# Kernel optimization log

Hardware: AMD Instinct MI355X
Metric: run time of the kernel (lower is better)

## Reference

```python
import jax, jax.numpy as jnp
import numpy as np


def setup_inputs() -> dict:
    key = jax.random.key(0)
    k1, k2 = jax.random.split(key)
    input_tensor = jax.random.normal(k1, (32, 128, 64, 64), dtype=jnp.float32)
    weights = jax.random.normal(k2, (256, 128, 3, 3), dtype=jnp.float32) * 0.05
    return {"input_tensor": input_tensor, "weights": weights}


def reference(input_tensor, weights):
    # Valid-padding, stride-1, no-bias direct conv2d (NCHW x OIHW -> NCHW),
    # identical math to the quintuple-loop slice*weight sum in the original.
    return jax.lax.conv_general_dilated(
        input_tensor,
        weights,
        window_strides=(1, 1),
        padding="VALID",
        dimension_numbers=("NCHW", "OIHW", "NCHW"),
    )
```

## Files before the change

kernel.cpp:

```cpp
#include <hip/hip_runtime.h>
#include <hip/hip_bf16.h>

#define N_IMG 32
#define CIN   128
#define INH   64
#define INW   64
#define COUT  256
#define OH    62
#define OW    62

typedef short          bf16x8 __attribute__((ext_vector_type(8)));
typedef unsigned short u16x8  __attribute__((ext_vector_type(8)));
typedef float          f32x4  __attribute__((ext_vector_type(4)));
typedef float          f32x2  __attribute__((ext_vector_type(2)));

__device__ __forceinline__ unsigned short f2bf(float x) {
    unsigned int u = __float_as_uint(x);
    u += 0x7fffu + ((u >> 16) & 1u);
    return (unsigned short)(u >> 16);
}

__device__ __forceinline__ void gload_lds16(const void* g, void* l) {
    __builtin_amdgcn_global_load_lds(
        (const __attribute__((address_space(1))) unsigned int*)g,
        (__attribute__((address_space(3))) unsigned int*)l, 16, 0, 0);
}

__global__ void wt_transform_kernel(const float* __restrict__ Wsrc,
                                    unsigned short* __restrict__ WT) {
    int idx = blockIdx.x * 256 + threadIdx.x;
    int i   = idx & 7;
    int co  = (idx >> 3) & 255;
    int cgk = idx >> 11;
    int cg  = cgk & 15;
    int khw = cgk >> 4;
    int kh  = khw / 3, kw = khw - 3 * kh;
    int ci  = cg * 8 + i;
    WT[idx] = f2bf(Wsrc[co * (CIN * 9) + ci * 9 + kh * 3 + kw]);
}

__global__ __launch_bounds__(256)
void in_transform_kernel(const float* __restrict__ In,
                         unsigned short* __restrict__ TIn) {
    __shared__ float T[32][66];
    const int bid = blockIdx.x;
    const int ih  = bid & 63;
    const int cb  = (bid >> 6) & 3;
    const int img = bid >> 8;

    {
        const int r  = threadIdx.x >> 3;
        const int c0 = (threadIdx.x & 7) * 8;
        const float* p = In + (((size_t)(img * CIN + cb * 32 + r)) * INH + ih) * INW + c0;
        f32x4 a = *(const f32x4*)p;
        f32x4 b = *(const f32x4*)(p + 4);
        *(f32x2*)&T[r][c0 + 0] = f32x2{a[0], a[1]};
        *(f32x2*)&T[r][c0 + 2] = f32x2{a[2], a[3]};
        *(f32x2*)&T[r][c0 + 4] = f32x2{b[0], b[1]};
        *(f32x2*)&T[r][c0 + 6] = f32x2{b[2], b[3]};
    }
    __syncthreads();

    const int c  = threadIdx.x;
    const int iw = c >> 2;
    const int cg = (c & 3) ^ ((iw >> 1) & 3);
    u16x8 v;
#pragma unroll
    for (int i = 0; i < 8; ++i) v[i] = f2bf(T[cg * 8 + i][iw]);
    *(u16x8*)&TIn[((size_t)bid * 256 + c) * 8] = v;
}

__global__ __launch_bounds__(256, 3)
void conv_mfma_bf16_kernel(const unsigned short* __restrict__ TIn,
                           const unsigned short* __restrict__ WT,
                           float* __restrict__ Out) {
    __shared__ unsigned short Lin[2][2112];

    const int g   = blockIdx.x;
    const int f   = (g & 7) * 248 + (g >> 3);
    const int img = f / OH;
    const int oh  = f - img * OH;

    const int tid  = threadIdx.x;
    const int wave = tid >> 6;
    const int lane = tid & 63;
    const int q    = lane >> 4;
    const int ml   = lane & 15;
    const int co_base = wave * 64;

    const unsigned short* tin_base = TIn + (size_t)img * (4 * 64 * 2048);
    const bf16x8* WTv = (const bf16x8*)WT;
    const int wlane = q * 256 + co_base + ml;

    int xoff[3][4];
#pragma unroll
    for (int kw = 0; kw < 3; ++kw)
#pragma unroll
        for (int ni = 0; ni < 4; ++ni) {
            const int r = ni * 16 + ml + kw;
            xoff[kw][ni] = r * 32 + ((q ^ ((r >> 1) & 3)) << 3);
        }

    f32x4 acc[4][4];
    const f32x4 zero = {0.f, 0.f, 0.f, 0.f};
#pragma unroll
    for (int a = 0; a < 4; ++a)
#pragma unroll
        for (int b = 0; b < 4; ++b) acc[a][b] = zero;

    gload_lds16(tin_base + oh * 2048 + tid * 8, &Lin[0][wave * 512]);
    if (tid < 64) ((unsigned int*)&Lin[tid >> 5][64 * 32])[tid & 31] = 0u;
    __syncthreads();

    for (int s = 0; s < 12; ++s) {
        const int cur = s & 1;
        if (s < 11) {
            const int s1 = s + 1;
            const unsigned short* src =
                tin_base + ((s1 & 3) * 64 + oh + (s1 >> 2)) * 2048;
            gload_lds16(src + tid * 8, &Lin[cur ^ 1][wave * 512]);
        }
        const int kh = s >> 2, cb = s & 3;
#pragma unroll
        for (int kw = 0; kw < 3; ++kw) {
            const int khw = kh * 3 + kw;
            const bf16x8* wbase = WTv + (khw * 16 + cb * 4) * 256;
            bf16x8 wf[4], xf[4];
#pragma unroll
            for (int mi = 0; mi < 4; ++mi)
                wf[mi] = wbase[wlane + mi * 16];
#pragma unroll
            for (int ni = 0; ni < 4; ++ni)
                xf[ni] = *(const bf16x8*)&Lin[cur][xoff[kw][ni]];
#pragma unroll
            for (int mi = 0; mi < 4; ++mi)
#pragma unroll
                for (int ni = 0; ni < 4; ++ni)
                    acc[mi][ni] = __builtin_amdgcn_mfma_f32_16x16x32_bf16(
                        wf[mi], xf[ni], acc[mi][ni], 0, 0, 0);
        }
        __syncthreads();
    }

#pragma unroll
    for (int mi = 0; mi < 4; ++mi) {
#pragma unroll
        for (int r = 0; r < 4; ++r) {
            const int co = co_base + mi * 16 + q * 4 + r;
            float* op = Out + ((img * COUT + co) * OH + oh) * OW;
#pragma unroll
            for (int ni = 0; ni < 4; ++ni) {
                const int ow = ni * 16 + ml;
                if (ow < OW) op[ow] = acc[mi][ni][r];
            }
        }
    }
}

__global__ __launch_bounds__(256, 2)
void conv_mfma_fp32_kernel(const float* __restrict__ In,
                           const unsigned short* __restrict__ WT,
                           float* __restrict__ Out) {
    __shared__ unsigned short Lin[66 * 32];

    const int oh   = blockIdx.x;
    const int img  = blockIdx.y;
    const int tid  = threadIdx.x;
    const int wave = tid >> 6;
    const int lane = tid & 63;
    const int q    = lane >> 4;
    const int ml   = lane & 15;
    const int co_base = wave * 64;

    f32x4 acc[4][4];
    const f32x4 zero = {0.f, 0.f, 0.f, 0.f};
#pragma unroll
    for (int a = 0; a < 4; ++a)
#pragma unroll
        for (int b = 0; b < 4; ++b) acc[a][b] = zero;

    if (tid < 32) ((unsigned int*)&Lin[64 * 32])[tid] = 0u;

    const int s_iw = tid & 63;
    const int s_cg = tid >> 6;
    const bf16x8* WTv = (const bf16x8*)WT;

    for (int kh = 0; kh < 3; ++kh) {
        const int ih = oh + kh;
        for (int cb = 0; cb < 4; ++cb) {
            const float* p = In + (((img * CIN + cb * 32 + s_cg * 8) * INH + ih) * INW + s_iw);
            u16x8 v;
#pragma unroll
            for (int i = 0; i < 8; ++i) v[i] = f2bf(p[i * (INH * INW)]);
            __syncthreads();
            *(u16x8*)&Lin[s_iw * 32 + ((s_cg ^ (s_iw & 3)) << 3)] = v;
            __syncthreads();

#pragma unroll
            for (int kw = 0; kw < 3; ++kw) {
                const int khw = kh * 3 + kw;
                bf16x8 wf[4], xf[4];
#pragma unroll
                for (int mi = 0; mi < 4; ++mi)
                    wf[mi] = WTv[(khw * 16 + cb * 4 + q) * 256 + co_base + mi * 16 + ml];
#pragma unroll
                for (int ni = 0; ni < 4; ++ni) {
                    const int row = ni * 16 + ml + kw;
                    xf[ni] = *(const bf16x8*)&Lin[row * 32 + ((q ^ (row & 3)) << 3)];
                }
#pragma unroll
                for (int mi = 0; mi < 4; ++mi)
#pragma unroll
                    for (int ni = 0; ni < 4; ++ni)
                        acc[mi][ni] = __builtin_amdgcn_mfma_f32_16x16x32_bf16(
                            wf[mi], xf[ni], acc[mi][ni], 0, 0, 0);
            }
        }
    }

#pragma unroll
    for (int mi = 0; mi < 4; ++mi) {
#pragma unroll
        for (int r = 0; r < 4; ++r) {
            const int co = co_base + mi * 16 + q * 4 + r;
            float* op = Out + ((img * COUT + co) * OH + oh) * OW;
#pragma unroll
            for (int ni = 0; ni < 4; ++ni) {
                const int ow = ni * 16 + ml;
                if (ow < OW) op[ow] = acc[mi][ni][r];
            }
        }
    }
}

__global__ void conv_naive_kernel(const float* __restrict__ In,
                                  const float* __restrict__ Wt,
                                  float* __restrict__ Out) {
    int idx = blockIdx.x * 256 + threadIdx.x;
    const int total = N_IMG * COUT * OH * OW;
    if (idx >= total) return;
    int ow = idx % OW; int t = idx / OW;
    int oh = t % OH;   t /= OH;
    int co = t % COUT; int img = t / COUT;
    float s = 0.f;
    for (int ci = 0; ci < CIN; ++ci)
#pragma unroll
        for (int kh = 0; kh < 3; ++kh)
#pragma unroll
            for (int kw = 0; kw < 3; ++kw)
                s += In[((img * CIN + ci) * INH + oh + kh) * INW + ow + kw] *
                     Wt[co * CIN * 9 + ci * 9 + kh * 3 + kw];
    Out[idx] = s;
}

extern "C" void kernel_launch(void* const* d_in, const int* in_sizes, int n_in,
                              void* d_out, int out_size, void* d_ws, size_t ws_size,
                              hipStream_t stream) {
    const float* In   = (const float*)d_in[0];
    const float* Wsrc = (const float*)d_in[1];
    float* Out        = (float*)d_out;

    const size_t WT_BYTES  = (size_t)9 * 16 * 256 * 8 * sizeof(unsigned short);
    const size_t TIN_BYTES = (size_t)N_IMG * 4 * 64 * 2048 * sizeof(unsigned short);

    if (ws_size >= WT_BYTES + TIN_BYTES) {
        unsigned short* WT  = (unsigned short*)d_ws;
        unsigned short* TIn = (unsigned short*)((char*)d_ws + WT_BYTES);
        wt_transform_kernel<<<dim3(294912 / 256), dim3(256), 0, stream>>>(Wsrc, WT);
        in_transform_kernel<<<dim3(N_IMG * 4 * 64), dim3(256), 0, stream>>>(In, TIn);
        conv_mfma_bf16_kernel<<<dim3(OH * N_IMG), dim3(256), 0, stream>>>(TIn, WT, Out);
    } else if (ws_size >= WT_BYTES) {
        unsigned short* WT = (unsigned short*)d_ws;
        wt_transform_kernel<<<dim3(294912 / 256), dim3(256), 0, stream>>>(Wsrc, WT);
        conv_mfma_fp32_kernel<<<dim3(OH, N_IMG), dim3(256), 0, stream>>>(In, WT, Out);
    } else {
        const int total = N_IMG * COUT * OH * OW;
        conv_naive_kernel<<<dim3((total + 255) / 256), dim3(256), 0, stream>>>(In, Wsrc, Out);
    }
}
```

Before: 251.9 us.

## Compute two output rows per block to reuse weight fragments and input rows

Each block now produces two adjacent output rows, loading four input rows per channel block into LDS and reusing each weight fragment load for both rows. The grid is halved to 992 blocks and the pipeline goes from 12 steps to 4 larger stages, which roughly halves global weight traffic per output and cuts per-block overheads. In exchange, the accumulators double to 128 floats per thread and LDS use quadruples, so launch bounds drop from 3 to 2 blocks per CU, lowering occupancy and latency hiding.

```diff
diff --git a/kernel.cpp b/kernel.cpp
--- a/kernel.cpp
+++ b/kernel.cpp
@@ -70,16 +70,17 @@
     *(u16x8*)&TIn[((size_t)bid * 256 + c) * 8] = v;
 }
 
-__global__ __launch_bounds__(256, 3)
+__global__ __launch_bounds__(256, 2)
 void conv_mfma_bf16_kernel(const unsigned short* __restrict__ TIn,
                            const unsigned short* __restrict__ WT,
                            float* __restrict__ Out) {
-    __shared__ unsigned short Lin[2][2112];
+    __shared__ unsigned short Lin[2][4][2112];
 
     const int g   = blockIdx.x;
-    const int f   = (g & 7) * 248 + (g >> 3);
-    const int img = f / OH;
-    const int oh  = f - img * OH;
+    const int f   = (g & 7) * 124 + (g >> 3);
+    const int img = f / 31;
+    const int ohp = f - img * 31;
+    const int oh  = ohp * 2;
 
     const int tid  = threadIdx.x;
     const int wave = tid >> 6;
@@ -101,60 +102,77 @@
             xoff[kw][ni] = r * 32 + ((q ^ ((r >> 1) & 3)) << 3);
         }
 
-    f32x4 acc[4][4];
+    f32x4 acc[2][4][4];
     const f32x4 zero = {0.f, 0.f, 0.f, 0.f};
 #pragma unroll
-    for (int a = 0; a < 4; ++a)
-#pragma unroll
-        for (int b = 0; b < 4; ++b) acc[a][b] = zero;
-
-    gload_lds16(tin_base + oh * 2048 + tid * 8, &Lin[0][wave * 512]);
-    if (tid < 64) ((unsigned int*)&Lin[tid >> 5][64 * 32])[tid & 31] = 0u;
+    for (int r = 0; r < 2; ++r)
+#pragma unroll
+        for (int a = 0; a < 4; ++a)
+#pragma unroll
+            for (int b = 0; b < 4; ++b) acc[r][a][b] = zero;
+
+    {
+        unsigned int* L = (unsigned int*)Lin;
+        const int rb = tid >> 5;
+        L[rb * 1056 + 1024 + (tid & 31)] = 0u;
+    }
+    for (int j = 0; j < 4; ++j)
+        gload_lds16(tin_base + (oh + j) * 2048 + tid * 8, &Lin[0][j][wave * 512]);
     __syncthreads();
 
-    for (int s = 0; s < 12; ++s) {
-        const int cur = s & 1;
-        if (s < 11) {
-            const int s1 = s + 1;
-            const unsigned short* src =
-                tin_base + ((s1 & 3) * 64 + oh + (s1 >> 2)) * 2048;
-            gload_lds16(src + tid * 8, &Lin[cur ^ 1][wave * 512]);
-        }
-        const int kh = s >> 2, cb = s & 3;
-#pragma unroll
-        for (int kw = 0; kw < 3; ++kw) {
-            const int khw = kh * 3 + kw;
-            const bf16x8* wbase = WTv + (khw * 16 + cb * 4) * 256;
-            bf16x8 wf[4], xf[4];
-#pragma unroll
-            for (int mi = 0; mi < 4; ++mi)
-                wf[mi] = wbase[wlane + mi * 16];
-#pragma unroll
-            for (int ni = 0; ni < 4; ++ni)
-                xf[ni] = *(const bf16x8*)&Lin[cur][xoff[kw][ni]];
-#pragma unroll
-            for (int mi = 0; mi < 4; ++mi)
-#pragma unroll
-                for (int ni = 0; ni < 4; ++ni)
-                    acc[mi][ni] = __builtin_amdgcn_mfma_f32_16x16x32_bf16(
-                        wf[mi], xf[ni], acc[mi][ni], 0, 0, 0);
+    int cur = 0;
+    for (int cb = 0; cb < 4; ++cb) {
+        if (cb < 3) {
+            const unsigned short* src = tin_base + ((cb + 1) * 64 + oh) * 2048;
+            for (int j = 0; j < 4; ++j)
+                gload_lds16(src + j * 2048 + tid * 8, &Lin[cur ^ 1][j][wave * 512]);
+        }
+#pragma unroll
+        for (int kh = 0; kh < 3; ++kh) {
+            bf16x8 wf[3][4];
+#pragma unroll
+            for (int kw = 0; kw < 3; ++kw) {
+                const bf16x8* wbase = WTv + ((kh * 3 + kw) * 16 + cb * 4) * 256;
+#pragma unroll
+                for (int mi = 0; mi < 4; ++mi)
+                    wf[kw][mi] = wbase[wlane + mi * 16];
+            }
+#pragma unroll
+            for (int r = 0; r < 2; ++r) {
+                const unsigned short* rowb = &Lin[cur][r + kh][0];
+#pragma unroll
+                for (int kw = 0; kw < 3; ++kw) {
+                    bf16x8 xf[4];
+#pragma unroll
+                    for (int ni = 0; ni < 4; ++ni)
+                        xf[ni] = *(const bf16x8*)&rowb[xoff[kw][ni]];
+#pragma unroll
+                    for (int mi = 0; mi < 4; ++mi)
+#pragma unroll
+                        for (int ni = 0; ni < 4; ++ni)
+                            acc[r][mi][ni] = __builtin_amdgcn_mfma_f32_16x16x32_bf16(
+                                wf[kw][mi], xf[ni], acc[r][mi][ni], 0, 0, 0);
+                }
+            }
         }
         __syncthreads();
-    }
-
-#pragma unroll
-    for (int mi = 0; mi < 4; ++mi) {
-#pragma unroll
-        for (int r = 0; r < 4; ++r) {
-            const int co = co_base + mi * 16 + q * 4 + r;
-            float* op = Out + ((img * COUT + co) * OH + oh) * OW;
-#pragma unroll
-            for (int ni = 0; ni < 4; ++ni) {
-                const int ow = ni * 16 + ml;
-                if (ow < OW) op[ow] = acc[mi][ni][r];
-            }
-        }
-    }
+        cur ^= 1;
+    }
+
+#pragma unroll
+    for (int r = 0; r < 2; ++r)
+#pragma unroll
+        for (int mi = 0; mi < 4; ++mi)
+#pragma unroll
+            for (int rr = 0; rr < 4; ++rr) {
+                const int co = co_base + mi * 16 + q * 4 + rr;
+                float* op = Out + ((img * COUT + co) * OH + oh + r) * OW;
+#pragma unroll
+                for (int ni = 0; ni < 4; ++ni) {
+                    const int ow = ni * 16 + ml;
+                    if (ow < OW) op[ow] = acc[r][mi][ni][rr];
+                }
+            }
 }
 
 __global__ __launch_bounds__(256, 2)
@@ -268,7 +286,7 @@
         unsigned short* TIn = (unsigned short*)((char*)d_ws + WT_BYTES);
         wt_transform_kernel<<<dim3(294912 / 256), dim3(256), 0, stream>>>(Wsrc, WT);
         in_transform_kernel<<<dim3(N_IMG * 4 * 64), dim3(256), 0, stream>>>(In, TIn);
-        conv_mfma_bf16_kernel<<<dim3(OH * N_IMG), dim3(256), 0, stream>>>(TIn, WT, Out);
+        conv_mfma_bf16_kernel<<<dim3(992), dim3(256), 0, stream>>>(TIn, WT, Out);
     } else if (ws_size >= WT_BYTES) {
         unsigned short* WT = (unsigned short*)d_ws;
         wt_transform_kernel<<<dim3(294912 / 256), dim3(256), 0, stream>>>(Wsrc, WT);
```

Measured after the change: 275.1 us. +9.2%, slower.
